# Kernel optimization log

Measured on AMD Instinct MI355X. Metric: run time of the kernel, lower is better.

Reference implementation:

```python
import jax, jax.numpy as jnp
from jax import lax
import numpy as np

VOCAB, EMBED, HID, MAXLEN, BATCH = 50000, 512, 1024, 100, 512
FORGET_BIAS = 2.0


def setup_inputs() -> dict:
    key = jax.random.key(0)
    ks = jax.random.split(key, 12)
    s = 0.02
    input_queries = jax.random.randint(ks[0], (BATCH, MAXLEN), 0, VOCAB, dtype=jnp.int32)
    input_replies = jax.random.randint(ks[1], (BATCH, MAXLEN), 0, VOCAB, dtype=jnp.int32)
    query_lengths = jnp.maximum(jax.random.randint(ks[2], (BATCH,), 0, MAXLEN, dtype=jnp.int32), 1)
    reply_lengths = jnp.maximum(jax.random.randint(ks[3], (BATCH,), 0, MAXLEN, dtype=jnp.int32), 1)
    embeddings = jax.random.normal(ks[4], (VOCAB, EMBED), dtype=jnp.float32) * s
    # shared peephole LSTM weights (reuse=True in the original): kernel over [x; h], gate order i, j, f, o
    W = jax.random.normal(ks[5], (EMBED + HID, 4 * HID), dtype=jnp.float32) * s
    b = jnp.zeros((4 * HID,), dtype=jnp.float32)
    p_i = jax.random.normal(ks[6], (HID,), dtype=jnp.float32) * s
    p_f = jax.random.normal(ks[7], (HID,), dtype=jnp.float32) * s
    p_o = jax.random.normal(ks[8], (HID,), dtype=jnp.float32) * s
    M = jax.random.normal(ks[9], (HID, HID), dtype=jnp.float32) * s
    return {
        "embeddings": embeddings, "W": W, "b": b,
        "p_i": p_i, "p_f": p_f, "p_o": p_o, "M": M,
        "input_queries": input_queries, "input_replies": input_replies,
        "query_lengths": query_lengths, "reply_lengths": reply_lengths,
    }


def _lstm_encode(x_emb, lengths, W, b, p_i, p_f, p_o):
    """Peephole LSTM (TF LSTMCell, use_peepholes=True). Returns final h at sequence_length."""
    B, L, _ = x_emb.shape
    H = p_i.shape[0]

    def step(carry, xt):
        c, h = carry
        x_t, t = xt                      # x_t: [B, E]
        z = jnp.concatenate([x_t, h], axis=-1) @ W + b   # [B, 4H]
        zi, zj, zf, zo = jnp.split(z, 4, axis=-1)
        i = jax.nn.sigmoid(zi + p_i * c)
        f = jax.nn.sigmoid(zf + FORGET_BIAS + p_f * c)
        c_new = f * c + i * jnp.tanh(zj)
        o = jax.nn.sigmoid(zo + p_o * c_new)
        h_new = o * jnp.tanh(c_new)
        valid = (t < lengths)[:, None]   # hold state past sequence_length
        return (jnp.where(valid, c_new, c), jnp.where(valid, h_new, h)), None

    init = (jnp.zeros((B, H), x_emb.dtype), jnp.zeros((B, H), x_emb.dtype))
    xs = (jnp.swapaxes(x_emb, 0, 1), jnp.arange(L, dtype=jnp.int32))
    (_, h), _ = lax.scan(step, init, xs)
    return h


def reference(embeddings, W, b, p_i, p_f, p_o, M,
              input_queries, input_replies, query_lengths, reply_lengths):
    q_emb = embeddings[input_queries]    # [B, L, E]
    r_emb = embeddings[input_replies]
    q_enc = _lstm_encode(q_emb, query_lengths, W, b, p_i, p_f, p_o)   # [B, H]
    r_enc = _lstm_encode(r_emb, reply_lengths, W, b, p_i, p_f, p_o)
    q_t = q_enc @ M                                                    # bilinear transform
    distances = q_t @ r_enc.T                                          # [B, B]
    # positives = diagonal, negatives = all off-diagonal (in-batch negatives)
    labels = jnp.eye(distances.shape[0], dtype=distances.dtype)
    # sigmoid cross entropy: softplus(x) - label * x, mean over all B*B logits
    loss = jnp.mean(jax.nn.softplus(distances) - labels * distances)
    return distances, loss
```

## Files before the change

kernel.cpp:

```cpp
#include <hip/hip_runtime.h>
#include <stdint.h>

typedef unsigned short u16;
typedef __bf16 bf16x8 __attribute__((ext_vector_type(8)));
typedef float f32x4 __attribute__((ext_vector_type(4)));

#define AS1 __attribute__((address_space(1)))
#define AS3 __attribute__((address_space(3)))

__device__ __forceinline__ void ld_lds16(const void* gp, void* lp) {
  __builtin_amdgcn_global_load_lds((AS1 void*)(void*)gp, (AS3 void*)lp, 16, 0, 0);
}

__device__ __forceinline__ u16 f2bf(float f) {
  uint32_t u = __float_as_uint(f);
  u += 0x7FFFu + ((u >> 16) & 1u);
  return (u16)(u >> 16);
}

__device__ __forceinline__ float fsig(float x) { return 1.0f / (1.0f + __expf(-x)); }
__device__ __forceinline__ float ftanhf(float x) {
  float e = __expf(-2.0f * fabsf(x));
  float t = (1.0f - e) / (1.0f + e);
  return copysignf(t, x);
}

#define LSEQ 100
#define EMB 512
#define HID 1024
#define KDIM 1536

__global__ __launch_bounds__(512, 2) void k_step(
    const u16* __restrict__ emb, const u16* __restrict__ W2T,
    const float* __restrict__ b2, const float* __restrict__ p_i,
    const float* __restrict__ p_f, const float* __restrict__ p_o,
    const int* __restrict__ tokQ, const int* __restrict__ tokR,
    const int* __restrict__ lenQ, const int* __restrict__ lenR,
    const u16* __restrict__ h_cur, u16* __restrict__ h_nxt,
    float* __restrict__ c_st, int t)
{
  __shared__ __align__(16) u16 sb[4 * 16384];
  const int tid = threadIdx.x;
  const int lane = tid & 63, wid = tid >> 6;
  const int kw = wid >> 2;
  const int wm = (wid >> 1) & 1, wn = wid & 1;
  const int lane_lo = lane & 15, lane_hi = lane >> 4;
  const int g = blockIdx.x;
  const int bx = (g & 7) * 4 + ((g >> 3) & 3);
  const int by = g >> 5;

  f32x4 acc[4][4];
  const f32x4 zz = {0.f, 0.f, 0.f, 0.f};
#pragma unroll
  for (int a = 0; a < 4; ++a)
#pragma unroll
    for (int bb = 0; bb < 4; ++bb) acc[a][bb] = zz;

  int tokv[2], rowe[2], rowi[2], ldsoA[2], srcoA[2];
#pragma unroll
  for (int j = 0; j < 2; ++j) {
    const int ch = j * 512 + tid;
    const int r = ch >> 3;
    const int srcoff = ((ch & 7) ^ (r & 7)) * 8;
    const int m = by * 128 + r, e = m >> 9, i = m & 511;
    tokv[j] = (e ? tokR : tokQ)[i * LSEQ + t];
    rowe[j] = e; rowi[j] = i;
    srcoA[j] = srcoff;
    ldsoA[j] = ch * 8;
  }

  const int colbase = bx * 128 + wn * 64;
  const int h = ((colbase >> 6) << 4) + lane_lo;
  const int mo = kw * 2;
  float b2v[4];
#pragma unroll
  for (int gg = 0; gg < 4; ++gg) b2v[gg] = b2[colbase + gg * 16 + lane_lo];
  const float pi = p_i[h], pf = p_f[h], po = p_o[h];
  int lenv[2][4];
  float cold[2][4];
  u16 hprev[2][4];
#pragma unroll
  for (int m2 = 0; m2 < 2; ++m2)
#pragma unroll
    for (int r = 0; r < 4; ++r) {
      const int m = by * 128 + wm * 64 + (mo + m2) * 16 + lane_hi * 4 + r;
      const int e = m >> 9, i = m & 511;
      lenv[m2][r] = e ? lenR[i] : lenQ[i];
      const size_t ci = (size_t)(e * 512 + i) * HID + h;
      cold[m2][r] = c_st[ci];
      hprev[m2][r] = h_cur[ci];
    }
  __builtin_amdgcn_sched_barrier(0);

  const u16* pAx[2];
  const u16* pAh[2];
  const u16* pB[2];
  int ldsoB[2];
#pragma unroll
  for (int j = 0; j < 2; ++j) {
    pAx[j] = emb + (size_t)tokv[j] * EMB + srcoA[j];
    pAh[j] = h_cur + (size_t)(rowe[j] * 512 + rowi[j]) * HID - 512 + srcoA[j];
  }
#pragma unroll
  for (int j = 0; j < 2; ++j) {
    const int ch = j * 512 + tid;
    const int r = ch >> 3;
    const int srcoff = ((ch & 7) ^ (r & 7)) * 8;
    pB[j] = W2T + (size_t)(bx * 128 + r) * KDIM + srcoff;
    ldsoB[j] = ch * 8;
  }

  auto stage = [&](int kt) {
    const int kb = kt * 64;
    u16* lA = sb + (kt & 3) * 16384;
    u16* lB = lA + 8192;
    const bool isx = kb < EMB;
#pragma unroll
    for (int j = 0; j < 2; ++j) ld_lds16((isx ? pAx[j] : pAh[j]) + kb, lA + ldsoA[j]);
#pragma unroll
    for (int j = 0; j < 2; ++j) ld_lds16(pB[j] + kb, lB + ldsoB[j]);
  };

  auto compute = [&](int buf) {
    const u16* lA = sb + buf * 16384;
    const u16* lB = lA + 8192;
    bf16x8 aF[4], bF[4];
#pragma unroll
    for (int mi = 0; mi < 4; ++mi) {
      const int rr = wm * 64 + mi * 16 + lane_lo;
      const int byo = rr * 128 + ((kw * 64 + lane_hi * 16) ^ ((rr & 7) << 4));
      aF[mi] = *(const bf16x8*)((const char*)lA + byo);
    }
#pragma unroll
    for (int ni = 0; ni < 4; ++ni) {
      const int rr = wn * 64 + ni * 16 + lane_lo;
      const int byo = rr * 128 + ((kw * 64 + lane_hi * 16) ^ ((rr & 7) << 4));
      bF[ni] = *(const bf16x8*)((const char*)lB + byo);
    }
#pragma unroll
    for (int mi = 0; mi < 4; ++mi)
#pragma unroll
      for (int ni = 0; ni < 4; ++ni)
        acc[mi][ni] = __builtin_amdgcn_mfma_f32_16x16x32_bf16(aF[mi], bF[ni], acc[mi][ni], 0, 0, 0);
  };

  stage(0);
  stage(1);
  stage(2);

  for (int kt = 0; kt < 24; ++kt) {
    if (kt < 22)       asm volatile("s_waitcnt vmcnt(8)" ::: "memory");
    else if (kt == 22) asm volatile("s_waitcnt vmcnt(4)" ::: "memory");
    else               asm volatile("s_waitcnt vmcnt(0)" ::: "memory");
    __builtin_amdgcn_s_barrier();
    __builtin_amdgcn_sched_barrier(0);
    if (kt < 21) stage(kt + 3);
    __builtin_amdgcn_s_setprio(1);
    compute(kt & 3);
    __builtin_amdgcn_s_setprio(0);
  }

  float* cmbf = (float*)sb;
  const int pair = wm * 2 + wn;
  {
    float* wslot = cmbf + (pair * 2 + kw) * 2048;
    if (kw == 0) {
#pragma unroll
      for (int m2 = 0; m2 < 2; ++m2)
#pragma unroll
        for (int ni = 0; ni < 4; ++ni)
          *(f32x4*)(wslot + (m2 * 4 + ni) * 256 + lane * 4) = acc[2 + m2][ni];
    } else {
#pragma unroll
      for (int m2 = 0; m2 < 2; ++m2)
#pragma unroll
        for (int ni = 0; ni < 4; ++ni)
          *(f32x4*)(wslot + (m2 * 4 + ni) * 256 + lane * 4) = acc[m2][ni];
    }
  }
  __syncthreads();
  f32x4 accF[2][4];
  {
    const float* rslot = cmbf + (pair * 2 + (kw ^ 1)) * 2048;
    if (kw == 0) {
#pragma unroll
      for (int m2 = 0; m2 < 2; ++m2)
#pragma unroll
        for (int ni = 0; ni < 4; ++ni)
          accF[m2][ni] = acc[m2][ni] + *(const f32x4*)(rslot + (m2 * 4 + ni) * 256 + lane * 4);
    } else {
#pragma unroll
      for (int m2 = 0; m2 < 2; ++m2)
#pragma unroll
        for (int ni = 0; ni < 4; ++ni)
          accF[m2][ni] = acc[2 + m2][ni] + *(const f32x4*)(rslot + (m2 * 4 + ni) * 256 + lane * 4);
    }
  }

#pragma unroll
  for (int m2 = 0; m2 < 2; ++m2) {
#pragma unroll
    for (int r = 0; r < 4; ++r) {
      const int m = by * 128 + wm * 64 + (mo + m2) * 16 + lane_hi * 4 + r;
      const int e = m >> 9, i = m & 511;
      const size_t ci = (size_t)(e * 512 + i) * HID + h;
      u16 hv;
      if (t < lenv[m2][r]) {
        const float c_old = cold[m2][r];
        const float zi = accF[m2][0][r] + b2v[0] + pi * c_old;
        const float zj = accF[m2][1][r] + b2v[1];
        const float zf = accF[m2][2][r] + b2v[2] + pf * c_old;
        const float zo = accF[m2][3][r] + b2v[3];
        const float ig = fsig(zi), fg = fsig(zf);
        const float cn = fg * c_old + ig * ftanhf(zj);
        const float og = fsig(zo + po * cn);
        const float hn = og * ftanhf(cn);
        c_st[ci] = cn;
        hv = f2bf(hn);
      } else {
        hv = hprev[m2][r];
      }
      h_nxt[ci] = hv;
    }
  }
}

template <int OUT_BF16>
__global__ __launch_bounds__(256) void k_gemm(
    const u16* __restrict__ A, const u16* __restrict__ Bn,
    void* __restrict__ Cout, int K, int ldc)
{
  __shared__ u16 lA[128 * 64];
  __shared__ u16 lB[128 * 64];
  const int tid = threadIdx.x;
  const int lane = tid & 63, wid = tid >> 6;
  const int wm = wid >> 1, wn = wid & 1;
  const int lane_lo = lane & 15, lane_hi = lane >> 4;
  const int bx = blockIdx.x, by = blockIdx.y;

  f32x4 acc[4][4];
  const f32x4 zz = {0.f, 0.f, 0.f, 0.f};
#pragma unroll
  for (int a = 0; a < 4; ++a)
#pragma unroll
    for (int bb = 0; bb < 4; ++bb) acc[a][bb] = zz;

  const int nkt = K >> 6;
  for (int kt = 0; kt < nkt; ++kt) {
    const int kb = kt * 64;
#pragma unroll
    for (int j = 0; j < 4; ++j) {
      const int cbase = (j * 4 + wid) * 64;
      const int ch = cbase + lane;
      const int r = ch >> 3;
      const int srcoff = ((((ch & 7) << 4) ^ ((r & 7) << 4)) >> 1);
      ld_lds16(A + (size_t)(by * 128 + r) * K + kb + srcoff, &lA[cbase * 8]);
    }
#pragma unroll
    for (int j = 0; j < 4; ++j) {
      const int cbase = (j * 4 + wid) * 64;
      const int ch = cbase + lane;
      const int r = ch >> 3;
      const int srcoff = ((((ch & 7) << 4) ^ ((r & 7) << 4)) >> 1);
      ld_lds16(Bn + (size_t)(bx * 128 + r) * K + kb + srcoff, &lB[cbase * 8]);
    }
    __syncthreads();
#pragma unroll
    for (int kk = 0; kk < 2; ++kk) {
      bf16x8 aF[4], bF[4];
#pragma unroll
      for (int mi = 0; mi < 4; ++mi) {
        const int rr = wm * 64 + mi * 16 + lane_lo;
        const int byo = rr * 128 + ((kk * 64 + lane_hi * 16) ^ ((rr & 7) << 4));
        aF[mi] = *(const bf16x8*)((const char*)lA + byo);
      }
#pragma unroll
      for (int ni = 0; ni < 4; ++ni) {
        const int rr = wn * 64 + ni * 16 + lane_lo;
        const int byo = rr * 128 + ((kk * 64 + lane_hi * 16) ^ ((rr & 7) << 4));
        bF[ni] = *(const bf16x8*)((const char*)lB + byo);
      }
#pragma unroll
      for (int mi = 0; mi < 4; ++mi)
#pragma unroll
        for (int ni = 0; ni < 4; ++ni)
          acc[mi][ni] = __builtin_amdgcn_mfma_f32_16x16x32_bf16(aF[mi], bF[ni], acc[mi][ni], 0, 0, 0);
    }
    __syncthreads();
  }

#pragma unroll
  for (int mi = 0; mi < 4; ++mi)
#pragma unroll
    for (int r = 0; r < 4; ++r) {
      const int m = by * 128 + wm * 64 + mi * 16 + lane_hi * 4 + r;
#pragma unroll
      for (int ni = 0; ni < 4; ++ni) {
        const int col = bx * 128 + wn * 64 + ni * 16 + lane_lo;
        const float v = acc[mi][ni][r];
        if (OUT_BF16) ((u16*)Cout)[(size_t)m * ldc + col] = f2bf(v);
        else ((float*)Cout)[(size_t)m * ldc + col] = v;
      }
    }
}

__global__ void k_transpose(const float* __restrict__ in, u16* __restrict__ out,
                            int K_, int N_, int perm)
{
  __shared__ float tile[64][65];
  const int tid = threadIdx.x;
  const int k0 = blockIdx.y * 64, n0 = blockIdx.x * 64;
  const int c = tid & 63, rq = tid >> 6;
  for (int rr = 0; rr < 64; rr += 4)
    tile[rr + rq][c] = in[(size_t)(k0 + rr + rq) * N_ + n0 + c];
  __syncthreads();
  for (int nr0 = 0; nr0 < 64; nr0 += 4) {
    const int nr = nr0 + rq;
    const int n = n0 + nr;
    int np = n;
    if (perm) {
      const int g = n >> 10, hh = n & 1023;
      np = ((hh >> 4) << 6) + (g << 4) + (hh & 15);
    }
    out[(size_t)np * K_ + k0 + c] = f2bf(tile[c][nr]);
  }
}

__global__ void k_bias(const float* __restrict__ b, float* __restrict__ b2) {
  const int n = blockIdx.x * 256 + threadIdx.x;
  if (n < 4096) {
    const int g = n >> 10, hh = n & 1023;
    const int np = ((hh >> 4) << 6) + (g << 4) + (hh & 15);
    b2[np] = b[n] + (g == 2 ? 2.0f : 0.0f);
  }
}

__global__ void k_cvt(const float4* __restrict__ in, u16* __restrict__ out, size_t n4) {
  size_t idx = (size_t)blockIdx.x * blockDim.x + threadIdx.x;
  const size_t stride = (size_t)gridDim.x * blockDim.x;
  for (; idx < n4; idx += stride) {
    const float4 v = in[idx];
    ushort4 o;
    o.x = f2bf(v.x); o.y = f2bf(v.y); o.z = f2bf(v.z); o.w = f2bf(v.w);
    *(ushort4*)(out + idx * 4) = o;
  }
}

__global__ void k_zero(uint4* __restrict__ p, size_t n) {
  size_t idx = (size_t)blockIdx.x * blockDim.x + threadIdx.x;
  const size_t stride = (size_t)gridDim.x * blockDim.x;
  const uint4 z = {0u, 0u, 0u, 0u};
  for (; idx < n; idx += stride) p[idx] = z;
}

__global__ void k_loss1(const float* __restrict__ D, float* __restrict__ part) {
  __shared__ float sd[256];
  const int tid = threadIdx.x;
  float s = 0.f;
  for (int idx = blockIdx.x * 256 + tid; idx < 512 * 512; idx += 256 * 256) {
    const float x = D[idx];
    float sp;
    if (x > 20.f) sp = x;
    else if (x < -20.f) sp = __expf(x);
    else sp = __logf(1.0f + __expf(x));
    if ((idx >> 9) == (idx & 511)) sp -= x;
    s += sp;
  }
  sd[tid] = s;
  __syncthreads();
  for (int o = 128; o > 0; o >>= 1) { if (tid < o) sd[tid] += sd[tid + o]; __syncthreads(); }
  if (tid == 0) part[blockIdx.x] = sd[0];
}

__global__ void k_loss2(const float* __restrict__ part, float* __restrict__ out) {
  __shared__ float sd[256];
  const int tid = threadIdx.x;
  sd[tid] = part[tid];
  __syncthreads();
  for (int o = 128; o > 0; o >>= 1) { if (tid < o) sd[tid] += sd[tid + o]; __syncthreads(); }
  if (tid == 0) out[0] = sd[0] * (1.0f / (512.0f * 512.0f));
}

extern "C" void kernel_launch(void* const* d_in, const int* in_sizes, int n_in,
                              void* d_out, int out_size, void* d_ws, size_t ws_size,
                              hipStream_t stream)
{
  const float* embF = (const float*)d_in[0];
  const float* W    = (const float*)d_in[1];
  const float* b    = (const float*)d_in[2];
  const float* p_i  = (const float*)d_in[3];
  const float* p_f  = (const float*)d_in[4];
  const float* p_o  = (const float*)d_in[5];
  const float* Mm   = (const float*)d_in[6];
  const int* tokQ   = (const int*)d_in[7];
  const int* tokR   = (const int*)d_in[8];
  const int* lenQ   = (const int*)d_in[9];
  const int* lenR   = (const int*)d_in[10];
  float* out = (float*)d_out;

  char* ws = (char*)d_ws;
  const size_t OFF_EMB  = 0;
  const size_t OFF_W2T  = 51200000;
  const size_t OFF_MT   = OFF_W2T + 12582912;
  const size_t OFF_B2   = OFF_MT + 2097152;
  const size_t OFF_H    = OFF_B2 + 16384;
  const size_t OFF_C    = OFF_H + 4194304;
  const size_t OFF_QT   = OFF_C + 4194304;
  const size_t OFF_PART = OFF_QT + 1048576;
  const size_t NEED = OFF_PART + 1024;
  if (ws_size < NEED) return;

  u16* embB  = (u16*)(ws + OFF_EMB);
  u16* W2T   = (u16*)(ws + OFF_W2T);
  u16* MT    = (u16*)(ws + OFF_MT);
  float* b2  = (float*)(ws + OFF_B2);
  u16* hbuf  = (u16*)(ws + OFF_H);
  float* cst = (float*)(ws + OFF_C);
  u16* qt    = (u16*)(ws + OFF_QT);
  float* part= (float*)(ws + OFF_PART);

  k_cvt<<<dim3(2048), dim3(256), 0, stream>>>((const float4*)embF, embB, (size_t)(50000 * 512 / 4));
  k_transpose<<<dim3(64, 24), dim3(256), 0, stream>>>(W, W2T, 1536, 4096, 1);
  k_transpose<<<dim3(16, 16), dim3(256), 0, stream>>>(Mm, MT, 1024, 1024, 0);
  k_bias<<<dim3(16), dim3(256), 0, stream>>>(b, b2);
  k_zero<<<dim3(256), dim3(256), 0, stream>>>((uint4*)hbuf, 131072);
  k_zero<<<dim3(256), dim3(256), 0, stream>>>((uint4*)cst, 262144);

  const size_t HBUFSTRIDE = (size_t)2 * 512 * 1024;
  for (int t = 0; t < 100; ++t) {
    u16* hc = hbuf + (size_t)(t & 1) * HBUFSTRIDE;
    u16* hn = hbuf + (size_t)((t + 1) & 1) * HBUFSTRIDE;
    k_step<<<dim3(256), dim3(512), 0, stream>>>(embB, W2T, b2, p_i, p_f, p_o,
                                                tokQ, tokR, lenQ, lenR, hc, hn, cst, t);
  }

  k_gemm<1><<<dim3(8, 4), dim3(256), 0, stream>>>(hbuf, MT, qt, 1024, 1024);
  k_gemm<0><<<dim3(4, 4), dim3(256), 0, stream>>>(qt, hbuf + (size_t)512 * 1024, out, 1024, 512);

  k_loss1<<<dim3(256), dim3(256), 0, stream>>>(out, part);
  k_loss2<<<dim3(1), dim3(256), 0, stream>>>(part, out + 262144);
}
```

Before: 2.078 ms.

## Pre-pack LSTM weights in MFMA fragment order and load B directly to registers

A new pack kernel writes the gate-permuted LSTM weight matrix in bf16, laid out in the exact per-lane MFMA fragment order for each wave. The step kernel then loads B fragments straight from global memory into registers, double-buffered one k-tile ahead, instead of staging B through LDS. Only the A operand (embeddings and hidden state) still goes through a 4-stage LDS ring, which halves shared memory use and removes B's LDS reads and writes. The risk is exposed global-load latency on B, since it is prefetched only one tile ahead and held in registers, which also raises register pressure.

```diff
diff --git a/kernel.cpp b/kernel.cpp
--- a/kernel.cpp
+++ b/kernel.cpp
@@ -31,7 +31,7 @@
 #define KDIM 1536
 
 __global__ __launch_bounds__(512, 2) void k_step(
-    const u16* __restrict__ emb, const u16* __restrict__ W2T,
+    const u16* __restrict__ emb, const u16* __restrict__ Wfm,
     const float* __restrict__ b2, const float* __restrict__ p_i,
     const float* __restrict__ p_f, const float* __restrict__ p_o,
     const int* __restrict__ tokQ, const int* __restrict__ tokR,
@@ -39,7 +39,7 @@
     const u16* __restrict__ h_cur, u16* __restrict__ h_nxt,
     float* __restrict__ c_st, int t)
 {
-  __shared__ __align__(16) u16 sb[4 * 16384];
+  __shared__ __align__(16) u16 sb[4 * 8192];
   const int tid = threadIdx.x;
   const int lane = tid & 63, wid = tid >> 6;
   const int kw = wid >> 2;
@@ -94,72 +94,71 @@
 
   const u16* pAx[2];
   const u16* pAh[2];
-  const u16* pB[2];
-  int ldsoB[2];
 #pragma unroll
   for (int j = 0; j < 2; ++j) {
     pAx[j] = emb + (size_t)tokv[j] * EMB + srcoA[j];
     pAh[j] = h_cur + (size_t)(rowe[j] * 512 + rowi[j]) * HID - 512 + srcoA[j];
   }
-#pragma unroll
-  for (int j = 0; j < 2; ++j) {
-    const int ch = j * 512 + tid;
-    const int r = ch >> 3;
-    const int srcoff = ((ch & 7) ^ (r & 7)) * 8;
-    pB[j] = W2T + (size_t)(bx * 128 + r) * KDIM + srcoff;
-    ldsoB[j] = ch * 8;
-  }
-
-  auto stage = [&](int kt) {
+  const u16* pWl = Wfm + (size_t)(((bx * 2 + wn) * 2) + kw) * 49152 + lane * 8;
+
+  auto stageA = [&](int kt) {
     const int kb = kt * 64;
-    u16* lA = sb + (kt & 3) * 16384;
-    u16* lB = lA + 8192;
+    u16* lA = sb + (kt & 3) * 8192;
     const bool isx = kb < EMB;
 #pragma unroll
     for (int j = 0; j < 2; ++j) ld_lds16((isx ? pAx[j] : pAh[j]) + kb, lA + ldsoA[j]);
-#pragma unroll
-    for (int j = 0; j < 2; ++j) ld_lds16(pB[j] + kb, lB + ldsoB[j]);
   };
 
-  auto compute = [&](int buf) {
-    const u16* lA = sb + buf * 16384;
-    const u16* lB = lA + 8192;
-    bf16x8 aF[4], bF[4];
+  auto loadB = [&](int kt, bf16x8 (&Bs)[4]) {
+    const u16* p = pWl + kt * 2048;
+#pragma unroll
+    for (int ni = 0; ni < 4; ++ni)
+      Bs[ni] = *(const bf16x8*)(p + ni * 512);
+  };
+
+  auto compute = [&](int kt, const bf16x8 (&Bs)[4]) {
+    const char* lA = (const char*)(sb + (kt & 3) * 8192);
+    bf16x8 aF[4];
 #pragma unroll
     for (int mi = 0; mi < 4; ++mi) {
       const int rr = wm * 64 + mi * 16 + lane_lo;
       const int byo = rr * 128 + ((kw * 64 + lane_hi * 16) ^ ((rr & 7) << 4));
-      aF[mi] = *(const bf16x8*)((const char*)lA + byo);
-    }
-#pragma unroll
-    for (int ni = 0; ni < 4; ++ni) {
-      const int rr = wn * 64 + ni * 16 + lane_lo;
-      const int byo = rr * 128 + ((kw * 64 + lane_hi * 16) ^ ((rr & 7) << 4));
-      bF[ni] = *(const bf16x8*)((const char*)lB + byo);
+      aF[mi] = *(const bf16x8*)(lA + byo);
     }
 #pragma unroll
     for (int mi = 0; mi < 4; ++mi)
 #pragma unroll
       for (int ni = 0; ni < 4; ++ni)
-        acc[mi][ni] = __builtin_amdgcn_mfma_f32_16x16x32_bf16(aF[mi], bF[ni], acc[mi][ni], 0, 0, 0);
+        acc[mi][ni] = __builtin_amdgcn_mfma_f32_16x16x32_bf16(aF[mi], Bs[ni], acc[mi][ni], 0, 0, 0);
   };
 
-  stage(0);
-  stage(1);
-  stage(2);
-
-  for (int kt = 0; kt < 24; ++kt) {
-    if (kt < 22)       asm volatile("s_waitcnt vmcnt(8)" ::: "memory");
-    else if (kt == 22) asm volatile("s_waitcnt vmcnt(4)" ::: "memory");
-    else               asm volatile("s_waitcnt vmcnt(0)" ::: "memory");
-    __builtin_amdgcn_s_barrier();
-    __builtin_amdgcn_sched_barrier(0);
-    if (kt < 21) stage(kt + 3);
-    __builtin_amdgcn_s_setprio(1);
-    compute(kt & 3);
-    __builtin_amdgcn_s_setprio(0);
-  }
-
+  bf16x8 B0[4], B1[4];
+
+  loadB(0, B0);
+  stageA(0); stageA(1); stageA(2);
+
+#define STEP_ITER(KT, BU, BF, VM)                                   \
+  asm volatile("s_waitcnt vmcnt(" #VM ")" ::: "memory");            \
+  __builtin_amdgcn_s_barrier();                                     \
+  __builtin_amdgcn_sched_barrier(0);                                \
+  if ((KT) < 23) loadB((KT) + 1, BF);                               \
+  if ((KT) < 21) stageA((KT) + 3);                                  \
+  __builtin_amdgcn_s_setprio(1);                                    \
+  compute((KT), BU);                                                \
+  __builtin_amdgcn_s_setprio(0);
+
+  STEP_ITER(0, B0, B1, 4)
+  STEP_ITER(1, B1, B0, 2)
+  for (int j = 1; j <= 10; ++j) {
+    const int kt = 2 * j;
+    STEP_ITER(kt, B0, B1, 2)
+    STEP_ITER(kt + 1, B1, B0, 2)
+  }
+  STEP_ITER(22, B0, B1, 0)
+  STEP_ITER(23, B1, B0, 0)
+#undef STEP_ITER
+
+  __syncthreads();
   float* cmbf = (float*)sb;
   const int pair = wm * 2 + wn;
   {
@@ -304,6 +303,36 @@
     }
 }
 
+__global__ void k_pack(const float* __restrict__ W, u16* __restrict__ Wfm) {
+  __shared__ float tile[64][65];
+  const int n0 = blockIdx.x * 64;
+  const int k0 = blockIdx.y * 64;
+  const int tid = threadIdx.x;
+  const int c = tid & 63, rq = tid >> 6;
+  for (int rr = 0; rr < 64; rr += 4)
+    tile[rr + rq][c] = W[(size_t)(k0 + rr + rq) * 4096 + n0 + c];
+  __syncthreads();
+  const int gate = n0 >> 10;
+  const int h0 = n0 & 1023;
+  const int kt = k0 >> 6;
+  for (int cc = tid; cc < 512; cc += 256) {
+    const int hh = cc >> 3;
+    const int k8 = cc & 7;
+    const int h = h0 + hh;
+    const int np = ((h >> 4) << 6) + (gate << 4) + (h & 15);
+    const int bx = np >> 7, wn = (np >> 6) & 1, ni = (np >> 4) & 3, llo = np & 15;
+    const int kw = k8 >> 2, lhi = k8 & 3;
+    const int lane = lhi * 16 + llo;
+    u16 oc[8];
+#pragma unroll
+    for (int e = 0; e < 8; ++e)
+      oc[e] = f2bf(tile[k8 * 8 + e][hh]);
+    const size_t o = ((((size_t)(bx * 2 + wn) * 2 + kw) * 24 + kt) * 4 + ni) * 512 + lane * 8;
+    *(ushort4*)(Wfm + o)     = *(ushort4*)&oc[0];
+    *(ushort4*)(Wfm + o + 4) = *(ushort4*)&oc[4];
+  }
+}
+
 __global__ void k_transpose(const float* __restrict__ in, u16* __restrict__ out,
                             int K_, int N_, int perm)
 {
@@ -400,8 +429,8 @@
 
   char* ws = (char*)d_ws;
   const size_t OFF_EMB  = 0;
-  const size_t OFF_W2T  = 51200000;
-  const size_t OFF_MT   = OFF_W2T + 12582912;
+  const size_t OFF_WFM  = 51200000;
+  const size_t OFF_MT   = OFF_WFM + 12582912;
   const size_t OFF_B2   = OFF_MT + 2097152;
   const size_t OFF_H    = OFF_B2 + 16384;
   const size_t OFF_C    = OFF_H + 4194304;
@@ -411,7 +440,7 @@
   if (ws_size < NEED) return;
 
   u16* embB  = (u16*)(ws + OFF_EMB);
-  u16* W2T   = (u16*)(ws + OFF_W2T);
+  u16* Wfm   = (u16*)(ws + OFF_WFM);
   u16* MT    = (u16*)(ws + OFF_MT);
   float* b2  = (float*)(ws + OFF_B2);
   u16* hbuf  = (u16*)(ws + OFF_H);
@@ -420,7 +449,7 @@
   float* part= (float*)(ws + OFF_PART);
 
   k_cvt<<<dim3(2048), dim3(256), 0, stream>>>((const float4*)embF, embB, (size_t)(50000 * 512 / 4));
-  k_transpose<<<dim3(64, 24), dim3(256), 0, stream>>>(W, W2T, 1536, 4096, 1);
+  k_pack<<<dim3(64, 24), dim3(256), 0, stream>>>(W, Wfm);
   k_transpose<<<dim3(16, 16), dim3(256), 0, stream>>>(Mm, MT, 1024, 1024, 0);
   k_bias<<<dim3(16), dim3(256), 0, stream>>>(b, b2);
   k_zero<<<dim3(256), dim3(256), 0, stream>>>((uint4*)hbuf, 131072);
@@ -430,7 +459,7 @@
   for (int t = 0; t < 100; ++t) {
     u16* hc = hbuf + (size_t)(t & 1) * HBUFSTRIDE;
     u16* hn = hbuf + (size_t)((t + 1) & 1) * HBUFSTRIDE;
-    k_step<<<dim3(256), dim3(512), 0, stream>>>(embB, W2T, b2, p_i, p_f, p_o,
+    k_step<<<dim3(256), dim3(512), 0, stream>>>(embB, Wfm, b2, p_i, p_f, p_o,
                                                 tokQ, tokR, lenQ, lenR, hc, hn, cst, t);
   }
 
```

Measured after the change: 2.400 ms. 1.15x slower.
